# Optimization experiments

Measured on AMD Instinct MI355X. Metric: run time of the kernel, lower is better.

## Reference

```python
import jax, jax.numpy as jnp
import numpy as np

B, C, H, W = 8, 512, 64, 64
IC = C // 2  # inter_channel


def setup_inputs() -> dict:
    key = jax.random.key(0)
    ks = jax.random.split(key, 10)
    s = 0.02
    return {
        "x": jax.random.normal(ks[0], (B, C, H, W), dtype=jnp.float32),
        "y": jax.random.normal(ks[1], (B, C, H, W), dtype=jnp.float32),
        "w_phi": jax.random.normal(ks[2], (IC, C), dtype=jnp.float32) * s,
        "b_phi": jnp.zeros((IC,), dtype=jnp.float32),
        "w_theta": jax.random.normal(ks[3], (IC, C), dtype=jnp.float32) * s,
        "b_theta": jnp.zeros((IC,), dtype=jnp.float32),
        "w_g": jax.random.normal(ks[4], (IC, C), dtype=jnp.float32) * s,
        "b_g": jnp.zeros((IC,), dtype=jnp.float32),
        "w_mask": jax.random.normal(ks[5], (C, IC), dtype=jnp.float32) * s,
        "b_mask": jnp.zeros((C,), dtype=jnp.float32),
    }


def _conv1x1(w, b, t):
    # t: [b, cin, h, w]; 1x1 conv == channel matmul
    return jnp.einsum('oc,bchw->bohw', w, t) + b[None, :, None, None]


def reference(x, y, w_phi, b_phi, w_theta, b_theta, w_g, b_g, w_mask, b_mask):
    b, c, h, w = x.shape
    ic = w_phi.shape[0]  # c // 2
    # Faithful to the torch code: conv outputs ic channels but is viewed as
    # (b, c, -1), so the sequence length is N = h*w//2 and feature dim is c.
    x_phi = _conv1x1(w_phi, b_phi, y).reshape(b, c, -1)              # [b, c, N]
    x_theta = _conv1x1(w_theta, b_theta, x).reshape(b, c, -1)
    x_theta = jnp.transpose(x_theta, (0, 2, 1))                      # [b, N, c]
    x_g = _conv1x1(w_g, b_g, x).reshape(b, c, -1)
    dict
    x_g = jnp.transpose(x_g, (0, 2, 1))                              # [b, N, c]
    scores = jnp.einsum('bnc,bcm->bnm', x_theta, x_phi)              # [b, N, N]
    attn = jax.nn.softmax(scores, axis=1)  # softmax over dim=1 (columns), as in torch
    out_nl = jnp.einsum('bnm,bmc->bnc', attn, x_g)                   # [b, N, c]
    out_nl = jnp.transpose(out_nl, (0, 2, 1)).reshape(b, ic, h, w)   # [b, ic, h, w]
    mask = _conv1x1(w_mask, b_mask, out_nl)                          # [b, c, h, w]
    return mask + x
```

## Files before the change

kernel.cpp:

```cpp
#include <hip/hip_runtime.h>
#include <hip/hip_bf16.h>


typedef __attribute__((ext_vector_type(8))) short short8;
typedef __attribute__((ext_vector_type(4))) short short4v;
typedef __attribute__((ext_vector_type(4))) float f32x4;

__device__ __forceinline__ short f2bf(float f) {
  union { __hip_bfloat16 h; short s; } u; u.h = __float2bfloat16(f); return u.s;
}
__device__ __forceinline__ float bf2f(short s) {
  union { short s; __hip_bfloat16 h; } u; u.s = s; return __bfloat162float(u.h);
}

__device__ __forceinline__ void async_ld16(const void* g, void* l) {
  __builtin_amdgcn_global_load_lds(
      (const __attribute__((address_space(1))) unsigned int*)(unsigned long long)g,
      (__attribute__((address_space(3))) unsigned int*)(unsigned int)(unsigned long long)l,
      16, 0, 0);
}

__device__ __forceinline__ short8 frag_sw(const short* Ds, int row, int q8)
{
  return *(const short8*)&Ds[row * 32 + (((q8 >> 3) ^ ((row >> 2) & 3)) << 3)];
}

__global__ __launch_bounds__(512, 4)
void ov_k(const short* __restrict__ Eg, const short* __restrict__ Gg,
          short* __restrict__ Cg)
{
  const int L = blockIdx.x;
  const int xcd = L & 7, k = L >> 3;
  const int slab = xcd + ((k >> 2) << 3);
  const int bz = slab >> 4, by = slab & 15, bx = k & 3;

  __shared__ __align__(16) short As[2][128 * 32];
  __shared__ __align__(16) short Bs[2][128 * 32];
  const short* A = Eg + ((long)bz << 22);
  const short* B = Gg + ((long)bz << 20);
  const int m0 = by * 128;
  const int n0 = bx * 128;
  const int t = threadIdx.x;
  const int wv = t >> 6, ln = t & 63;
  const int wr = wv >> 1, wc = wv & 1;
  const int fr = ln & 15, q8 = (ln >> 4) * 8;
  const int rowA = t >> 2;
  const int kcs = ((t & 3) ^ ((t >> 4) & 3)) * 8;

  f32x4 acc[2][4];
  #pragma unroll
  for (int i = 0; i < 2; i++)
    #pragma unroll
    for (int j = 0; j < 4; j++)
      #pragma unroll
      for (int r = 0; r < 4; r++) acc[i][j][r] = 0.f;

  async_ld16(A + (long)(m0 + rowA) * 2048 + kcs, &As[0][0] + wv * 512);
  async_ld16(B + (long)(n0 + rowA) * 2048 + kcs, &Bs[0][0] + wv * 512);
  __syncthreads();

  for (int kt = 1; kt < 64; kt++) {
    const int cur = (kt - 1) & 1, nxt = kt & 1;
    async_ld16(A + (long)(m0 + rowA) * 2048 + kt * 32 + kcs, &As[nxt][0] + wv * 512);
    async_ld16(B + (long)(n0 + rowA) * 2048 + kt * 32 + kcs, &Bs[nxt][0] + wv * 512);
    short8 af[2], bfr[4];
    #pragma unroll
    for (int mi = 0; mi < 2; mi++) af[mi] = frag_sw(&As[cur][0], wr * 32 + mi * 16 + fr, q8);
    #pragma unroll
    for (int ni = 0; ni < 4; ni++) bfr[ni] = frag_sw(&Bs[cur][0], wc * 64 + ni * 16 + fr, q8);
    #pragma unroll
    for (int mi = 0; mi < 2; mi++)
      #pragma unroll
      for (int ni = 0; ni < 4; ni++)
        acc[mi][ni] = __builtin_amdgcn_mfma_f32_16x16x32_bf16(af[mi], bfr[ni], acc[mi][ni], 0, 0, 0);
    __syncthreads();
  }
  {
    short8 af[2], bfr[4];
    #pragma unroll
    for (int mi = 0; mi < 2; mi++) af[mi] = frag_sw(&As[1][0], wr * 32 + mi * 16 + fr, q8);
    #pragma unroll
    for (int ni = 0; ni < 4; ni++) bfr[ni] = frag_sw(&Bs[1][0], wc * 64 + ni * 16 + fr, q8);
    #pragma unroll
    for (int mi = 0; mi < 2; mi++)
      #pragma unroll
      for (int ni = 0; ni < 4; ni++)
        acc[mi][ni] = __builtin_amdgcn_mfma_f32_16x16x32_bf16(af[mi], bfr[ni], acc[mi][ni], 0, 0, 0);
  }

  const int colb = n0 + wc * 64 + fr;
  const int rowb = m0 + wr * 32 + (ln >> 4) * 4;
  #pragma unroll
  for (int mi = 0; mi < 2; mi++)
    #pragma unroll
    for (int r = 0; r < 4; r++) {
      const int mr = rowb + mi * 16 + r;
      #pragma unroll
      for (int ni = 0; ni < 4; ni++)
        Cg[((long)bz << 20) + (long)mr * 512 + colb + ni * 16] = f2bf(acc[mi][ni][r]);
    }
}

__global__ __launch_bounds__(512, 4)
void conv_ptf(const float* __restrict__ x, const float* __restrict__ y,
              const short* __restrict__ wth, const short* __restrict__ wph,
              const float* __restrict__ bth, const float* __restrict__ bph,
              short* __restrict__ TPT2)
{
  __shared__ __align__(16) short As[2][128 * 32];
  __shared__ __align__(16) short Bs[2][256 * 32];
  const int slab = blockIdx.x;
  const bool isphi = slab >= 256;
  const int s2 = slab & 255;
  const float* src = (isphi ? y : x) + (long)(s2 >> 5) * (512L * 4096);
  const int px0 = (s2 & 31) * 128;
  const long m0 = (long)slab * 128;
  const short* W = isphi ? wph : wth;
  const float* bias = isphi ? bph : bth;
  const int t = threadIdx.x;
  const int wv = t >> 6, ln = t & 63;
  const int wpx = wv >> 2, wic = wv & 3;
  const int fr = ln & 15, q8 = (ln >> 4) * 8;
  const int g4 = (t >> 5) * 4, p4 = (t & 31) * 4;
  const int w2 = wv - 4;
  const int kcs = ((ln & 3) ^ (ln >> 4)) * 8;

  f32x4 acc[4][4];
  #pragma unroll
  for (int i = 0; i < 4; i++)
    #pragma unroll
    for (int j = 0; j < 4; j++)
      #pragma unroll
      for (int r = 0; r < 4; r++) acc[i][j][r] = 0.f;

  if (t >= 256) {
    #pragma unroll
    for (int j = 0; j < 4; j++)
      async_ld16(W + (long)(w2 * 64 + j * 16 + (ln >> 2)) * 512 + kcs,
                 &Bs[0][(w2 * 64 + j * 16) * 32]);
  } else {
    f32x4 r[4];
    #pragma unroll
    for (int i = 0; i < 4; i++)
      r[i] = *(const f32x4*)&src[(long)(g4 + i) * 4096 + px0 + p4];
    #pragma unroll
    for (int j = 0; j < 4; j++) {
      short4v w;
      w[0] = f2bf(r[0][j]); w[1] = f2bf(r[1][j]); w[2] = f2bf(r[2][j]); w[3] = f2bf(r[3][j]);
      const int px = p4 + j;
      const int u = (g4 >> 3) ^ ((px >> 2) & 3);
      *(short4v*)&As[0][px * 32 + u * 8 + (g4 & 4)] = w;
    }
  }
  __syncthreads();

  for (int k = 1; k < 16; k++) {
    const int cur = (k - 1) & 1, nxt = k & 1;
    f32x4 r[4];
    if (t >= 256) {
      #pragma unroll
      for (int j = 0; j < 4; j++)
        async_ld16(W + (long)(w2 * 64 + j * 16 + (ln >> 2)) * 512 + k * 32 + kcs,
                   &Bs[nxt][(w2 * 64 + j * 16) * 32]);
    } else {
      #pragma unroll
      for (int i = 0; i < 4; i++)
        r[i] = *(const f32x4*)&src[(long)(k * 32 + g4 + i) * 4096 + px0 + p4];
    }
    short8 af[4], bfv[4];
    #pragma unroll
    for (int mi = 0; mi < 4; mi++) af[mi] = frag_sw(&As[cur][0], wpx * 64 + mi * 16 + fr, q8);
    #pragma unroll
    for (int ni = 0; ni < 4; ni++) bfv[ni] = frag_sw(&Bs[cur][0], wic * 64 + ni * 16 + fr, q8);
    #pragma unroll
    for (int mi = 0; mi < 4; mi++)
      #pragma unroll
      for (int ni = 0; ni < 4; ni++)
        acc[mi][ni] = __builtin_amdgcn_mfma_f32_16x16x32_bf16(af[mi], bfv[ni], acc[mi][ni], 0, 0, 0);
    if (t < 256) {
      #pragma unroll
      for (int j = 0; j < 4; j++) {
        short4v w;
        w[0] = f2bf(r[0][j]); w[1] = f2bf(r[1][j]); w[2] = f2bf(r[2][j]); w[3] = f2bf(r[3][j]);
        const int px = p4 + j;
        const int u = (g4 >> 3) ^ ((px >> 2) & 3);
        *(short4v*)&As[nxt][px * 32 + u * 8 + (g4 & 4)] = w;
      }
    }
    __syncthreads();
  }

  {
    short8 af[4], bfv[4];
    #pragma unroll
    for (int mi = 0; mi < 4; mi++) af[mi] = frag_sw(&As[1][0], wpx * 64 + mi * 16 + fr, q8);
    #pragma unroll
    for (int ni = 0; ni < 4; ni++) bfv[ni] = frag_sw(&Bs[1][0], wic * 64 + ni * 16 + fr, q8);
    #pragma unroll
    for (int mi = 0; mi < 4; mi++)
      #pragma unroll
      for (int ni = 0; ni < 4; ni++)
        acc[mi][ni] = __builtin_amdgcn_mfma_f32_16x16x32_bf16(af[mi], bfv[ni], acc[mi][ni], 0, 0, 0);
  }

  const int colic = wic * 64 + fr;
  float cb[4];
  #pragma unroll
  for (int ni = 0; ni < 4; ni++) cb[ni] = bias[colic + ni * 16];
  #pragma unroll
  for (int mi = 0; mi < 4; mi++)
    #pragma unroll
    for (int r = 0; r < 4; r++) {
      const long m = m0 + wpx * 64 + mi * 16 + (ln >> 4) * 4 + r;
      #pragma unroll
      for (int ni = 0; ni < 4; ni++)
        TPT2[m * 256 + colic + ni * 16] = f2bf(acc[mi][ni][r] + cb[ni]);
    }
}

__global__ __launch_bounds__(512, 4)
void gemmG_f(const float* __restrict__ x, const short* __restrict__ wg,
             const float* __restrict__ bg, short* __restrict__ G)
{
  __shared__ __align__(16) short As[2][256 * 32];
  __shared__ __align__(16) short Bs[2][128 * 32];
  const int img = blockIdx.y;
  const int n0 = blockIdx.x * 128;
  const float* src = x + (long)img * 512 * 4096;
  const int t = threadIdx.x;
  const int wv = t >> 6, ln = t & 63;
  const int wr = wv >> 1, wc = wv & 1;
  const int fr = ln & 15, q8 = (ln >> 4) * 8;
  const int g4 = (t >> 5) * 4, p4 = (t & 31) * 4;
  const int w2 = wv - 4;
  const int kcs = ((ln & 3) ^ (ln >> 4)) * 8;

  f32x4 acc[4][4];
  #pragma unroll
  for (int i = 0; i < 4; i++)
    #pragma unroll
    for (int j = 0; j < 4; j++)
      #pragma unroll
      for (int r = 0; r < 4; r++) acc[i][j][r] = 0.f;

  if (t >= 256) {
    #pragma unroll
    for (int j = 0; j < 4; j++)
      async_ld16(wg + (long)(w2 * 64 + j * 16 + (ln >> 2)) * 512 + kcs,
                 &As[0][(w2 * 64 + j * 16) * 32]);
  } else {
    f32x4 r[4];
    #pragma unroll
    for (int i = 0; i < 4; i++)
      r[i] = *(const f32x4*)&src[(long)(g4 + i) * 4096 + n0 + p4];
    #pragma unroll
    for (int j = 0; j < 4; j++) {
      short4v w;
      w[0] = f2bf(r[0][j]); w[1] = f2bf(r[1][j]); w[2] = f2bf(r[2][j]); w[3] = f2bf(r[3][j]);
      const int px = p4 + j;
      const int u = (g4 >> 3) ^ ((px >> 2) & 3);
      *(short4v*)&Bs[0][px * 32 + u * 8 + (g4 & 4)] = w;
    }
  }
  __syncthreads();

  for (int k = 1; k < 16; k++) {
    const int cur = (k - 1) & 1, nxt = k & 1;
    f32x4 r[4];
    if (t >= 256) {
      #pragma unroll
      for (int j = 0; j < 4; j++)
        async_ld16(wg + (long)(w2 * 64 + j * 16 + (ln >> 2)) * 512 + k * 32 + kcs,
                   &As[nxt][(w2 * 64 + j * 16) * 32]);
    } else {
      #pragma unroll
      for (int i = 0; i < 4; i++)
        r[i] = *(const f32x4*)&src[(long)(k * 32 + g4 + i) * 4096 + n0 + p4];
    }
    short8 af[4], bfv[4];
    #pragma unroll
    for (int mi = 0; mi < 4; mi++) af[mi] = frag_sw(&As[cur][0], wr * 64 + mi * 16 + fr, q8);
    #pragma unroll
    for (int ni = 0; ni < 4; ni++) bfv[ni] = frag_sw(&Bs[cur][0], wc * 64 + ni * 16 + fr, q8);
    #pragma unroll
    for (int mi = 0; mi < 4; mi++)
      #pragma unroll
      for (int ni = 0; ni < 4; ni++)
        acc[mi][ni] = __builtin_amdgcn_mfma_f32_16x16x32_bf16(af[mi], bfv[ni], acc[mi][ni], 0, 0, 0);
    if (t < 256) {
      #pragma unroll
      for (int j = 0; j < 4; j++) {
        short4v w;
        w[0] = f2bf(r[0][j]); w[1] = f2bf(r[1][j]); w[2] = f2bf(r[2][j]); w[3] = f2bf(r[3][j]);
        const int px = p4 + j;
        const int u = (g4 >> 3) ^ ((px >> 2) & 3);
        *(short4v*)&Bs[nxt][px * 32 + u * 8 + (g4 & 4)] = w;
      }
    }
    __syncthreads();
  }

  {
    short8 af[4], bfv[4];
    #pragma unroll
    for (int mi = 0; mi < 4; mi++) af[mi] = frag_sw(&As[1][0], wr * 64 + mi * 16 + fr, q8);
    #pragma unroll
    for (int ni = 0; ni < 4; ni++) bfv[ni] = frag_sw(&Bs[1][0], wc * 64 + ni * 16 + fr, q8);
    #pragma unroll
    for (int mi = 0; mi < 4; mi++)
      #pragma unroll
      for (int ni = 0; ni < 4; ni++)
        acc[mi][ni] = __builtin_amdgcn_mfma_f32_16x16x32_bf16(af[mi], bfv[ni], acc[mi][ni], 0, 0, 0);
  }

  const int colb = n0 + wc * 64 + fr;
  const int rowb = wr * 64 + (ln >> 4) * 4;
  #pragma unroll
  for (int mi = 0; mi < 4; mi++)
    #pragma unroll
    for (int r = 0; r < 4; r++) {
      const int mr = rowb + mi * 16 + r;
      const float badd = bg[mr];
      #pragma unroll
      for (int ni = 0; ni < 4; ni++)
        G[((long)img << 20) + (long)mr * 4096 + colb + ni * 16] = f2bf(acc[mi][ni][r] + badd);
    }
}

__global__ __launch_bounds__(256)
void scores_k(const short* __restrict__ TT2, const short* __restrict__ PT2,
              short* __restrict__ ST, float* __restrict__ pstats)
{
  __shared__ __align__(16) short As[2][128 * 32];
  __shared__ __align__(16) short Bs[2][128 * 32];
  const int bz = blockIdx.z, by = blockIdx.y, bx = blockIdx.x;
  const int t = threadIdx.x;
  const int wv = t >> 6, ln = t & 63;
  const int wm = (wv >> 1) * 64, wn = (wv & 1) * 64;
  const int fr = ln & 15, q8 = (ln >> 4) * 8;
  const int rowA = t >> 2;
  const int kcs = ((t & 3) ^ ((t >> 4) & 3)) * 8;

  const short* Abase = TT2 + ((long)(bz * 4096 + by * 128)) * 256;
  const short* Bbase = PT2 + ((long)(bz * 4096 + bx * 128)) * 256;

  f32x4 acc[4][4];
  #pragma unroll
  for (int i = 0; i < 4; i++)
    #pragma unroll
    for (int j = 0; j < 4; j++)
      #pragma unroll
      for (int r = 0; r < 4; r++) acc[i][j][r] = 0.f;

  #define SC_STAGE(s, buf)                                                     \
    {                                                                          \
      const long hoff = (long)((s) >> 3) * 2048 * 256;                         \
      const int kk = ((s) & 7) * 32;                                           \
      _Pragma("unroll")                                                        \
      for (int sv = 0; sv < 2; sv++) {                                         \
        async_ld16(Abase + hoff + (long)(sv * 64 + rowA) * 256 + kk + kcs,     \
                   &As[buf][0] + (sv * 256 + wv * 64) * 8);                    \
        async_ld16(Bbase + hoff + (long)(sv * 64 + rowA) * 256 + kk + kcs,     \
                   &Bs[buf][0] + (sv * 256 + wv * 64) * 8);                    \
      }                                                                        \
    }

  SC_STAGE(0, 0);
  __syncthreads();
  for (int s = 1; s < 16; s++) {
    const int cur = (s - 1) & 1, nxt = s & 1;
    SC_STAGE(s, nxt);
    short8 af[4], bfr[4];
    #pragma unroll
    for (int mi = 0; mi < 4; mi++) af[mi] = frag_sw(&As[cur][0], wm + mi * 16 + fr, q8);
    #pragma unroll
    for (int ni = 0; ni < 4; ni++) bfr[ni] = frag_sw(&Bs[cur][0], wn + ni * 16 + fr, q8);
    #pragma unroll
    for (int mi = 0; mi < 4; mi++)
      #pragma unroll
      for (int ni = 0; ni < 4; ni++)
        acc[mi][ni] = __builtin_amdgcn_mfma_f32_16x16x32_bf16(af[mi], bfr[ni], acc[mi][ni], 0, 0, 0);
    __syncthreads();
  }
  {
    short8 af[4], bfr[4];
    #pragma unroll
    for (int mi = 0; mi < 4; mi++) af[mi] = frag_sw(&As[1][0], wm + mi * 16 + fr, q8);
    #pragma unroll
    for (int ni = 0; ni < 4; ni++) bfr[ni] = frag_sw(&Bs[1][0], wn + ni * 16 + fr, q8);
    #pragma unroll
    for (int mi = 0; mi < 4; mi++)
      #pragma unroll
      for (int ni = 0; ni < 4; ni++)
        acc[mi][ni] = __builtin_amdgcn_mfma_f32_16x16x32_bf16(af[mi], bfr[ni], acc[mi][ni], 0, 0, 0);
  }
  #undef SC_STAGE

  const int colb = bx * 128 + wn + fr;
  const int rowb = by * 128 + wm + (ln >> 4) * 4;
  short* base = ST + ((long)bz << 22);
  float ps[4] = {0.f, 0.f, 0.f, 0.f};
  #pragma unroll
  for (int mi = 0; mi < 4; mi++)
    #pragma unroll
    for (int r = 0; r < 4; r++) {
      const long mr = rowb + mi * 16 + r;
      #pragma unroll
      for (int ni = 0; ni < 4; ni++) {
        float e = __expf(acc[mi][ni][r]);
        base[mr * 2048 + colb + ni * 16] = f2bf(e);
        ps[ni] += e;
      }
    }
  #pragma unroll
  for (int ni = 0; ni < 4; ni++) {
    ps[ni] += __shfl_xor(ps[ni], 16);
    ps[ni] += __shfl_xor(ps[ni], 32);
  }
  float* part = (float*)&As[0][0];
  if (ln < 16) {
    #pragma unroll
    for (int ni = 0; ni < 4; ni++)
      part[(wv >> 1) * 128 + wn + ni * 16 + fr] = ps[ni];
  }
  __syncthreads();
  if (t < 128)
    pstats[((long)(bz * 16 + by)) * 2048 + bx * 128 + t] = part[t] + part[128 + t];
}

__global__ __launch_bounds__(256)
void zfinal(const float* __restrict__ pstats, float* __restrict__ invZ)
{
  const int g = blockIdx.x * 256 + threadIdx.x;
  const int b = g >> 11, col = g & 2047;
  float S = 0.f;
  #pragma unroll
  for (int rc = 0; rc < 16; rc++) S += pstats[((long)(b * 16 + rc)) * 2048 + col];
  invZ[g] = 1.f / S;
}

__global__ __launch_bounds__(256)
void g_scale(short* __restrict__ G, const float* __restrict__ invZ)
{
  const long base = ((long)blockIdx.x * 256 + threadIdx.x) * 8;
  const int bz = (int)(base >> 20);
  const int n2 = (int)(base & 4095);
  const float* z = invZ + bz * 2048 + (n2 & 2047);
  short8 v = *(short8*)&G[base];
  f32x4 z0 = *(const f32x4*)z;
  f32x4 z1 = *(const f32x4*)(z + 4);
  #pragma unroll
  for (int j = 0; j < 4; j++) { v[j] = f2bf(bf2f(v[j]) * z0[j]); v[4 + j] = f2bf(bf2f(v[4 + j]) * z1[j]); }
  *(short8*)&G[base] = v;
}

__global__ __launch_bounds__(256)
void mask_k(const short* __restrict__ Wm20, const short* __restrict__ Wm21,
            const short* __restrict__ OVT, const float* __restrict__ bmask,
            const float* __restrict__ x, float* __restrict__ out)
{
  __shared__ __align__(16) short As[2][128 * 32];
  __shared__ __align__(16) short Bs[2][128 * 32];
  const int bz = blockIdx.z;
  const int n0 = blockIdx.x * 128;
  const int m0 = blockIdx.y * 128;
  const short* A = (n0 >= 2048) ? Wm21 : Wm20;
  const short* B = OVT + ((long)bz << 20) + (long)(n0 & 2047) * 512;
  const int t = threadIdx.x;
  const int wv = t >> 6, ln = t & 63;
  const int wm = (wv >> 1) * 64, wn = (wv & 1) * 64;
  const int fr = ln & 15, q8 = (ln >> 4) * 8;
  const int rowA = t >> 2;
  const int kcs = ((t & 3) ^ ((t >> 4) & 3)) * 8;

  f32x4 acc[4][4];
  #pragma unroll
  for (int i = 0; i < 4; i++)
    #pragma unroll
    for (int j = 0; j < 4; j++)
      #pragma unroll
      for (int r = 0; r < 4; r++) acc[i][j][r] = 0.f;

  #define MK_STAGE(s, buf)                                                     \
    {                                                                          \
      const int kk = (s) * 32;                                                 \
      _Pragma("unroll")                                                        \
      for (int sv = 0; sv < 2; sv++) {                                         \
        async_ld16(A + (long)(m0 + sv * 64 + rowA) * 512 + kk + kcs,           \
                   &As[buf][0] + (sv * 256 + wv * 64) * 8);                    \
        async_ld16(B + (long)(sv * 64 + rowA) * 512 + kk + kcs,                \
                   &Bs[buf][0] + (sv * 256 + wv * 64) * 8);                    \
      }                                                                        \
    }

  MK_STAGE(0, 0);
  __syncthreads();
  for (int s = 1; s < 16; s++) {
    const int cur = (s - 1) & 1, nxt = s & 1;
    MK_STAGE(s, nxt);
    short8 af[4], bfr[4];
    #pragma unroll
    for (int mi = 0; mi < 4; mi++) af[mi] = frag_sw(&As[cur][0], wm + mi * 16 + fr, q8);
    #pragma unroll
    for (int ni = 0; ni < 4; ni++) bfr[ni] = frag_sw(&Bs[cur][0], wn + ni * 16 + fr, q8);
    #pragma unroll
    for (int mi = 0; mi < 4; mi++)
      #pragma unroll
      for (int ni = 0; ni < 4; ni++)
        acc[mi][ni] = __builtin_amdgcn_mfma_f32_16x16x32_bf16(af[mi], bfr[ni], acc[mi][ni], 0, 0, 0);
    __syncthreads();
  }
  {
    short8 af[4], bfr[4];
    #pragma unroll
    for (int mi = 0; mi < 4; mi++) af[mi] = frag_sw(&As[1][0], wm + mi * 16 + fr, q8);
    #pragma unroll
    for (int ni = 0; ni < 4; ni++) bfr[ni] = frag_sw(&Bs[1][0], wn + ni * 16 + fr, q8);
    #pragma unroll
    for (int mi = 0; mi < 4; mi++)
      #pragma unroll
      for (int ni = 0; ni < 4; ni++)
        acc[mi][ni] = __builtin_amdgcn_mfma_f32_16x16x32_bf16(af[mi], bfr[ni], acc[mi][ni], 0, 0, 0);
  }
  #undef MK_STAGE

  const int colb = n0 + wn + fr;
  const int rowb = m0 + wm + (ln >> 4) * 4;
  #pragma unroll
  for (int mi = 0; mi < 4; mi++)
    #pragma unroll
    for (int r = 0; r < 4; r++) {
      const int mr = rowb + mi * 16 + r;
      const float badd = bmask[mr];
      const long rbase = ((long)bz * 512 + mr) * 4096;
      #pragma unroll
      for (int ni = 0; ni < 4; ni++) {
        const int cc = colb + ni * 16;
        out[rbase + cc] = acc[mi][ni][r] + badd + x[rbase + cc];
      }
    }
}

__global__ __launch_bounds__(256)
void wconv2(const float* w_phi, const float* w_theta, const float* w_g,
            const float* w_mask,
            short* wph, short* wth, short* wg, short* Wm20, short* Wm21)
{
  const int seg = blockIdx.x >> 6;
  const int blk = blockIdx.x & 63;
  const int i0 = blk * 2048 + threadIdx.x * 8;
  if (seg < 3) {
    const float* s = seg == 0 ? w_phi : seg == 1 ? w_theta : w_g;
    short* d = seg == 0 ? wph : seg == 1 ? wth : wg;
    f32x4 a = *(const f32x4*)&s[i0];
    f32x4 b = *(const f32x4*)&s[i0 + 4];
    short8 o;
    #pragma unroll
    for (int j = 0; j < 4; j++) { o[j] = f2bf(a[j]); o[4 + j] = f2bf(b[j]); }
    *(short8*)&d[i0] = o;
  } else {
    const int o = i0 >> 8;
    f32x4 a = *(const f32x4*)&w_mask[i0];
    f32x4 b = *(const f32x4*)&w_mask[i0 + 4];
    short v[8];
    #pragma unroll
    for (int j = 0; j < 4; j++) { v[j] = f2bf(a[j]); v[4 + j] = f2bf(b[j]); }
    short8 a0, a1, b0, b1;
    #pragma unroll
    for (int j = 0; j < 4; j++) {
      a0[2 * j] = v[j];     a0[2 * j + 1] = 0;
      a1[2 * j] = v[4 + j]; a1[2 * j + 1] = 0;
      b0[2 * j] = 0;        b0[2 * j + 1] = v[j];
      b1[2 * j] = 0;        b1[2 * j + 1] = v[4 + j];
    }
    const long base = (long)o * 512 + 2 * (i0 & 255);
    *(short8*)&Wm20[base] = a0; *(short8*)&Wm20[base + 8] = a1;
    *(short8*)&Wm21[base] = b0; *(short8*)&Wm21[base + 8] = b1;
  }
}

extern "C" void kernel_launch(void* const* d_in, const int* in_sizes, int n_in,
                              void* d_out, int out_size, void* d_ws, size_t ws_size,
                              hipStream_t stream)
{
  (void)in_sizes; (void)n_in; (void)out_size; (void)ws_size;
  const float* x       = (const float*)d_in[0];
  const float* y       = (const float*)d_in[1];
  const float* w_phi   = (const float*)d_in[2];
  const float* b_phi   = (const float*)d_in[3];
  const float* w_theta = (const float*)d_in[4];
  const float* b_theta = (const float*)d_in[5];
  const float* w_g     = (const float*)d_in[6];
  const float* b_g     = (const float*)d_in[7];
  const float* w_mask  = (const float*)d_in[8];
  const float* b_mask  = (const float*)d_in[9];
  float* out = (float*)d_out;

  char* ws = (char*)d_ws;
  const long MB = 1L << 20;
  short* wph  = (short*)(ws + 0);
  short* wth  = (short*)(ws + 256 * 1024);
  short* wg   = (short*)(ws + 512 * 1024);
  short* Wm20 = (short*)(ws + 768 * 1024);
  short* Wm21 = (short*)(ws + 1280 * 1024);
  short* TPT2 = (short*)(ws + 66 * MB);
  short* G    = (short*)(ws + 98 * MB);
  short* ST   = (short*)(ws + 2 * MB);
  float* pstats = (float*)(ws + 114 * MB);
  float* invZ   = (float*)(ws + 115 * MB);
  short* OVT  = (short*)(ws + 66 * MB);

  dim3 blk(256, 1, 1);
  dim3 blk8(512, 1, 1);

  wconv2<<<dim3(256, 1, 1), blk, 0, stream>>>(w_phi, w_theta, w_g, w_mask,
                                              wph, wth, wg, Wm20, Wm21);

  conv_ptf<<<dim3(512, 1, 1), blk8, 0, stream>>>(x, y, wth, wph, b_theta, b_phi, TPT2);

  gemmG_f<<<dim3(32, 8, 1), blk8, 0, stream>>>(x, wg, b_g, G);

  scores_k<<<dim3(16, 16, 8), blk, 0, stream>>>(TPT2, TPT2 + 32768L * 256, ST, pstats);
  zfinal<<<dim3(64, 1, 1), blk, 0, stream>>>(pstats, invZ);
  g_scale<<<dim3(4096, 1, 1), blk, 0, stream>>>(G, invZ);

  ov_k<<<dim3(512, 1, 1), blk8, 0, stream>>>(ST, G, OVT);

  mask_k<<<dim3(32, 4, 8), blk, 0, stream>>>(Wm20, Wm21, OVT, b_mask, x, out);
}
```

Measured before the change: 361.4 us.

## Fuse g-projection GEMM into theta/phi conv kernel to share x loads

Removes the separate gemmG_f kernel and computes the g 1x1 conv inside the theta blocks of the theta/phi conv kernel. Those blocks already hold the bf16 x tile in LDS, so x is read from global memory and converted once instead of twice. In exchange, theta blocks do twice the MFMA work and keep a second accumulator set, which raises register and LDS use. Launch bounds drop from 4 to 2 blocks per CU, and phi blocks finish earlier than theta blocks, so the load across blocks is uneven.

```diff
diff --git a/kernel.cpp b/kernel.cpp
--- a/kernel.cpp
+++ b/kernel.cpp
@@ -101,18 +101,23 @@
     }
 }
 
-__global__ __launch_bounds__(512, 4)
-void conv_ptf(const float* __restrict__ x, const float* __restrict__ y,
+__global__ __launch_bounds__(512, 2)
+void conv_ptg(const float* __restrict__ x, const float* __restrict__ y,
               const short* __restrict__ wth, const short* __restrict__ wph,
+              const short* __restrict__ wg,
               const float* __restrict__ bth, const float* __restrict__ bph,
-              short* __restrict__ TPT2)
+              const float* __restrict__ bg,
+              short* __restrict__ TPT2, short* __restrict__ G)
 {
   __shared__ __align__(16) short As[2][128 * 32];
   __shared__ __align__(16) short Bs[2][256 * 32];
+  __shared__ __align__(16) short Cs[2][256 * 32];
   const int slab = blockIdx.x;
   const bool isphi = slab >= 256;
+  const bool doG = !isphi;
   const int s2 = slab & 255;
-  const float* src = (isphi ? y : x) + (long)(s2 >> 5) * (512L * 4096);
+  const int img = s2 >> 5;
+  const float* src = (isphi ? y : x) + (long)img * (512L * 4096);
   const int px0 = (s2 & 31) * 128;
   const long m0 = (long)slab * 128;
   const short* W = isphi ? wph : wth;
@@ -125,19 +130,25 @@
   const int w2 = wv - 4;
   const int kcs = ((ln & 3) ^ (ln >> 4)) * 8;
 
-  f32x4 acc[4][4];
+  f32x4 acc[4][4], accg[4][4];
   #pragma unroll
   for (int i = 0; i < 4; i++)
     #pragma unroll
     for (int j = 0; j < 4; j++)
       #pragma unroll
-      for (int r = 0; r < 4; r++) acc[i][j][r] = 0.f;
+      for (int r = 0; r < 4; r++) { acc[i][j][r] = 0.f; accg[i][j][r] = 0.f; }
 
   if (t >= 256) {
     #pragma unroll
     for (int j = 0; j < 4; j++)
       async_ld16(W + (long)(w2 * 64 + j * 16 + (ln >> 2)) * 512 + kcs,
                  &Bs[0][(w2 * 64 + j * 16) * 32]);
+    if (doG) {
+      #pragma unroll
+      for (int j = 0; j < 4; j++)
+        async_ld16(wg + (long)(w2 * 64 + j * 16 + (ln >> 2)) * 512 + kcs,
+                   &Cs[0][(w2 * 64 + j * 16) * 32]);
+    }
   } else {
     f32x4 r[4];
     #pragma unroll
@@ -162,6 +173,12 @@
       for (int j = 0; j < 4; j++)
         async_ld16(W + (long)(w2 * 64 + j * 16 + (ln >> 2)) * 512 + k * 32 + kcs,
                    &Bs[nxt][(w2 * 64 + j * 16) * 32]);
+      if (doG) {
+        #pragma unroll
+        for (int j = 0; j < 4; j++)
+          async_ld16(wg + (long)(w2 * 64 + j * 16 + (ln >> 2)) * 512 + k * 32 + kcs,
+                     &Cs[nxt][(w2 * 64 + j * 16) * 32]);
+      }
     } else {
       #pragma unroll
       for (int i = 0; i < 4; i++)
@@ -177,6 +194,18 @@
       #pragma unroll
       for (int ni = 0; ni < 4; ni++)
         acc[mi][ni] = __builtin_amdgcn_mfma_f32_16x16x32_bf16(af[mi], bfv[ni], acc[mi][ni], 0, 0, 0);
+    if (doG) {
+      short8 ag[4], bg2[4];
+      #pragma unroll
+      for (int mi = 0; mi < 4; mi++) ag[mi] = frag_sw(&Cs[cur][0], wic * 64 + mi * 16 + fr, q8);
+      #pragma unroll
+      for (int ni = 0; ni < 4; ni++) bg2[ni] = frag_sw(&As[cur][0], wpx * 64 + ni * 16 + fr, q8);
+      #pragma unroll
+      for (int mi = 0; mi < 4; mi++)
+        #pragma unroll
+        for (int ni = 0; ni < 4; ni++)
+          accg[mi][ni] = __builtin_amdgcn_mfma_f32_16x16x32_bf16(ag[mi], bg2[ni], accg[mi][ni], 0, 0, 0);
+    }
     if (t < 256) {
       #pragma unroll
       for (int j = 0; j < 4; j++) {
@@ -201,6 +230,18 @@
       #pragma unroll
       for (int ni = 0; ni < 4; ni++)
         acc[mi][ni] = __builtin_amdgcn_mfma_f32_16x16x32_bf16(af[mi], bfv[ni], acc[mi][ni], 0, 0, 0);
+    if (doG) {
+      short8 ag[4], bg2[4];
+      #pragma unroll
+      for (int mi = 0; mi < 4; mi++) ag[mi] = frag_sw(&Cs[1][0], wic * 64 + mi * 16 + fr, q8);
+      #pragma unroll
+      for (int ni = 0; ni < 4; ni++) bg2[ni] = frag_sw(&As[1][0], wpx * 64 + ni * 16 + fr, q8);
+      #pragma unroll
+      for (int mi = 0; mi < 4; mi++)
+        #pragma unroll
+        for (int ni = 0; ni < 4; ni++)
+          accg[mi][ni] = __builtin_amdgcn_mfma_f32_16x16x32_bf16(ag[mi], bg2[ni], accg[mi][ni], 0, 0, 0);
+    }
   }
 
   const int colic = wic * 64 + fr;
@@ -216,115 +257,20 @@
       for (int ni = 0; ni < 4; ni++)
         TPT2[m * 256 + colic + ni * 16] = f2bf(acc[mi][ni][r] + cb[ni]);
     }
-}
-
-__global__ __launch_bounds__(512, 4)
-void gemmG_f(const float* __restrict__ x, const short* __restrict__ wg,
-             const float* __restrict__ bg, short* __restrict__ G)
-{
-  __shared__ __align__(16) short As[2][256 * 32];
-  __shared__ __align__(16) short Bs[2][128 * 32];
-  const int img = blockIdx.y;
-  const int n0 = blockIdx.x * 128;
-  const float* src = x + (long)img * 512 * 4096;
-  const int t = threadIdx.x;
-  const int wv = t >> 6, ln = t & 63;
-  const int wr = wv >> 1, wc = wv & 1;
-  const int fr = ln & 15, q8 = (ln >> 4) * 8;
-  const int g4 = (t >> 5) * 4, p4 = (t & 31) * 4;
-  const int w2 = wv - 4;
-  const int kcs = ((ln & 3) ^ (ln >> 4)) * 8;
-
-  f32x4 acc[4][4];
-  #pragma unroll
-  for (int i = 0; i < 4; i++)
-    #pragma unroll
-    for (int j = 0; j < 4; j++)
-      #pragma unroll
-      for (int r = 0; r < 4; r++) acc[i][j][r] = 0.f;
-
-  if (t >= 256) {
-    #pragma unroll
-    for (int j = 0; j < 4; j++)
-      async_ld16(wg + (long)(w2 * 64 + j * 16 + (ln >> 2)) * 512 + kcs,
-                 &As[0][(w2 * 64 + j * 16) * 32]);
-  } else {
-    f32x4 r[4];
-    #pragma unroll
-    for (int i = 0; i < 4; i++)
-      r[i] = *(const f32x4*)&src[(long)(g4 + i) * 4096 + n0 + p4];
-    #pragma unroll
-    for (int j = 0; j < 4; j++) {
-      short4v w;
-      w[0] = f2bf(r[0][j]); w[1] = f2bf(r[1][j]); w[2] = f2bf(r[2][j]); w[3] = f2bf(r[3][j]);
-      const int px = p4 + j;
-      const int u = (g4 >> 3) ^ ((px >> 2) & 3);
-      *(short4v*)&Bs[0][px * 32 + u * 8 + (g4 & 4)] = w;
-    }
-  }
-  __syncthreads();
-
-  for (int k = 1; k < 16; k++) {
-    const int cur = (k - 1) & 1, nxt = k & 1;
-    f32x4 r[4];
-    if (t >= 256) {
-      #pragma unroll
-      for (int j = 0; j < 4; j++)
-        async_ld16(wg + (long)(w2 * 64 + j * 16 + (ln >> 2)) * 512 + k * 32 + kcs,
-                   &As[nxt][(w2 * 64 + j * 16) * 32]);
-    } else {
-      #pragma unroll
-      for (int i = 0; i < 4; i++)
-        r[i] = *(const f32x4*)&src[(long)(k * 32 + g4 + i) * 4096 + n0 + p4];
-    }
-    short8 af[4], bfv[4];
-    #pragma unroll
-    for (int mi = 0; mi < 4; mi++) af[mi] = frag_sw(&As[cur][0], wr * 64 + mi * 16 + fr, q8);
-    #pragma unroll
-    for (int ni = 0; ni < 4; ni++) bfv[ni] = frag_sw(&Bs[cur][0], wc * 64 + ni * 16 + fr, q8);
-    #pragma unroll
-    for (int mi = 0; mi < 4; mi++)
-      #pragma unroll
-      for (int ni = 0; ni < 4; ni++)
-        acc[mi][ni] = __builtin_amdgcn_mfma_f32_16x16x32_bf16(af[mi], bfv[ni], acc[mi][ni], 0, 0, 0);
-    if (t < 256) {
-      #pragma unroll
-      for (int j = 0; j < 4; j++) {
-        short4v w;
-        w[0] = f2bf(r[0][j]); w[1] = f2bf(r[1][j]); w[2] = f2bf(r[2][j]); w[3] = f2bf(r[3][j]);
-        const int px = p4 + j;
-        const int u = (g4 >> 3) ^ ((px >> 2) & 3);
-        *(short4v*)&Bs[nxt][px * 32 + u * 8 + (g4 & 4)] = w;
+
+  if (doG) {
+    const int colpx = px0 + wpx * 64 + fr;
+    #pragma unroll
+    for (int mi = 0; mi < 4; mi++)
+      #pragma unroll
+      for (int r = 0; r < 4; r++) {
+        const int ic = wic * 64 + mi * 16 + (ln >> 4) * 4 + r;
+        const float badd = bg[ic];
+        #pragma unroll
+        for (int ni = 0; ni < 4; ni++)
+          G[((long)img << 20) + (long)ic * 4096 + colpx + ni * 16] = f2bf(accg[mi][ni][r] + badd);
       }
-    }
-    __syncthreads();
-  }
-
-  {
-    short8 af[4], bfv[4];
-    #pragma unroll
-    for (int mi = 0; mi < 4; mi++) af[mi] = frag_sw(&As[1][0], wr * 64 + mi * 16 + fr, q8);
-    #pragma unroll
-    for (int ni = 0; ni < 4; ni++) bfv[ni] = frag_sw(&Bs[1][0], wc * 64 + ni * 16 + fr, q8);
-    #pragma unroll
-    for (int mi = 0; mi < 4; mi++)
-      #pragma unroll
-      for (int ni = 0; ni < 4; ni++)
-        acc[mi][ni] = __builtin_amdgcn_mfma_f32_16x16x32_bf16(af[mi], bfv[ni], acc[mi][ni], 0, 0, 0);
-  }
-
-  const int colb = n0 + wc * 64 + fr;
-  const int rowb = wr * 64 + (ln >> 4) * 4;
-  #pragma unroll
-  for (int mi = 0; mi < 4; mi++)
-    #pragma unroll
-    for (int r = 0; r < 4; r++) {
-      const int mr = rowb + mi * 16 + r;
-      const float badd = bg[mr];
-      #pragma unroll
-      for (int ni = 0; ni < 4; ni++)
-        G[((long)img << 20) + (long)mr * 4096 + colb + ni * 16] = f2bf(acc[mi][ni][r] + badd);
-    }
+  }
 }
 
 __global__ __launch_bounds__(256)
@@ -616,9 +562,8 @@
   wconv2<<<dim3(256, 1, 1), blk, 0, stream>>>(w_phi, w_theta, w_g, w_mask,
                                               wph, wth, wg, Wm20, Wm21);
 
-  conv_ptf<<<dim3(512, 1, 1), blk8, 0, stream>>>(x, y, wth, wph, b_theta, b_phi, TPT2);
-
-  gemmG_f<<<dim3(32, 8, 1), blk8, 0, stream>>>(x, wg, b_g, G);
+  conv_ptg<<<dim3(512, 1, 1), blk8, 0, stream>>>(x, y, wth, wph, wg,
+                                                 b_theta, b_phi, b_g, TPT2, G);
 
   scores_k<<<dim3(16, 16, 8), blk, 0, stream>>>(TPT2, TPT2 + 32768L * 256, ST, pstats);
   zfinal<<<dim3(64, 1, 1), blk, 0, stream>>>(pstats, invZ);
```

After: 372.3 us. 1.03x slower.
